# Optimization experiments

Hardware: AMD Instinct MI355X
Metric: run time of the kernel (lower is better)

Reference implementation:

```python
import jax, jax.numpy as jnp
import numpy as np
from jax import lax

B, T, E, H = 4096, 200, 64, 64
N_USER, N_ITEM = 100000, 100000
ATT_H1, ATT_H2 = 80, 40  # DIN attention MLP sizes
FCN_IN = 4 * E + H  # user + item + hist_sum + item*hist_sum + gru2 final state


def setup_inputs() -> dict:
    key = jax.random.key(0)
    ks = jax.random.split(key, 32)
    s = 0.1
    rn = lambda k, shp: (jax.random.normal(k, shp, dtype=jnp.float32) * s)
    u = jax.random.randint(ks[0], (B,), 0, N_USER)
    i = jax.random.randint(ks[1], (B,), 0, N_ITEM)
    hist_i = jax.random.randint(ks[2], (B, T), 0, N_ITEM)
    sl = jax.random.randint(ks[3], (B,), 1, T + 1)
    mask = (jnp.arange(T)[None, :] < sl[:, None]).astype(jnp.float32)
    inp = dict(u=u, i=i, hist_i=hist_i, mask=mask)
    inp.update(
        item_emb_w=rn(ks[4], (N_ITEM, E)),
        user_emb_w=rn(ks[5], (N_USER, E)),
        # GRU1 (input dim E, hidden H): gates [r,z] fused, candidate separate (TF GRUCell layout)
        gru1_Wg=rn(ks[6], (E, 2 * H)), gru1_Ug=rn(ks[7], (H, 2 * H)), gru1_bg=jnp.zeros((2 * H,), jnp.float32),
        gru1_Wc=rn(ks[8], (E, H)), gru1_Uc=rn(ks[9], (H, H)), gru1_bc=jnp.zeros((H,), jnp.float32),
        # DIN attention MLP over [q, k, q-k, q*k]
        Wa1=rn(ks[10], (4 * H, ATT_H1)), ba1=jnp.zeros((ATT_H1,), jnp.float32),
        Wa2=rn(ks[11], (ATT_H1, ATT_H2)), ba2=jnp.zeros((ATT_H2,), jnp.float32),
        Wa3=rn(ks[12], (ATT_H2, 1)), ba3=jnp.zeros((1,), jnp.float32),
        # GRU2 (input dim H, hidden H)
        gru2_Wg=rn(ks[13], (H, 2 * H)), gru2_Ug=rn(ks[14], (H, 2 * H)), gru2_bg=jnp.zeros((2 * H,), jnp.float32),
        gru2_Wc=rn(ks[15], (H, H)), gru2_Uc=rn(ks[16], (H, H)), gru2_bc=jnp.zeros((H,), jnp.float32),
        # fcn_net: dense(2E) -> prelu -> dense(40) -> prelu -> dense(1)
        W1=rn(ks[17], (FCN_IN, 2 * E)), b1=jnp.zeros((2 * E,), jnp.float32), p1=jnp.full((2 * E,), 0.25, jnp.float32),
        W2=rn(ks[18], (2 * E, 40)), b2=jnp.zeros((40,), jnp.float32), p2=jnp.full((40,), 0.25, jnp.float32),
        W3=rn(ks[19], (40, 1)), b3=jnp.zeros((1,), jnp.float32),
    )
    return inp


def _gru(x, mask, Wg, Ug, bg, Wc, Uc, bc):
    """TF GRUCell semantics; mask freezes state past sequence length. x: [B,T,D]."""
    xg = jnp.einsum('btd,dh->bth', x, Wg) + bg  # precompute input projections
    xc = jnp.einsum('btd,dh->bth', x, Wc) + bc
    h0 = jnp.zeros((x.shape[0], Uc.shape[0]), dtype=x.dtype)

    def step(h, inp):
        xg_t, xc_t, m = inp
        r, z = jnp.split(jax.nn.sigmoid(xg_t + h @ Ug), 2, axis=-1)
        c = jnp.tanh(xc_t + (r * h) @ Uc)
        h_new = z * h + (1.0 - z) * c
        h = m[:, None] * h_new + (1.0 - m[:, None]) * h
        return h, h

    hT, hs = lax.scan(step, h0, (xg.transpose(1, 0, 2), xc.transpose(1, 0, 2), mask.T))
    return jnp.transpose(hs, (1, 0, 2)), hT  # [B,T,H], [B,H]


def _prelu(x, a):
    return jnp.where(x >= 0, x, a * x)


def reference(u, i, hist_i, mask, item_emb_w, user_emb_w,
              gru1_Wg, gru1_Ug, gru1_bg, gru1_Wc, gru1_Uc, gru1_bc,
              Wa1, ba1, Wa2, ba2, Wa3, ba3,
              gru2_Wg, gru2_Ug, gru2_bg, gru2_Wc, gru2_Uc, gru2_bc,
              W1, b1, p1, W2, b2, p2, W3, b3):
    item_eb = item_emb_w[i]            # [B,E]
    user_eb = user_emb_w[u]            # [B,E]
    hist_eb = item_emb_w[hist_i]       # [B,T,E]
    hist_sum = jnp.sum(hist_eb, axis=1)  # original uses unmasked reduce_sum

    # GRU encoder over history
    rnn1, _ = _gru(hist_eb, mask, gru1_Wg, gru1_Ug, gru1_bg, gru1_Wc, gru1_Uc, gru1_bc)

    # DIN-style attention: target item queries GRU1 states
    q = jnp.broadcast_to(item_eb[:, None, :], rnn1.shape)  # [B,T,H] (E==H)
    din = jnp.concatenate([q, rnn1, q - rnn1, q * rnn1], axis=-1)  # [B,T,4H]
    d1 = jax.nn.sigmoid(din @ Wa1 + ba1)
    d2 = jax.nn.sigmoid(d1 @ Wa2 + ba2)
    scores = (d2 @ Wa3 + ba3)[..., 0]  # [B,T]
    scores = jnp.where(mask > 0, scores, -1e9)
    alpha = jax.nn.softmax(scores, axis=-1)  # [B,T]

    # second GRU over attention-weighted states
    att_in = rnn1 * alpha[..., None]
    _, final2 = _gru(att_in, mask, gru2_Wg, gru2_Ug, gru2_bg, gru2_Wc, gru2_Uc, gru2_bc)

    # fcn_net on concatenated features
    inp = jnp.concatenate([user_eb, item_eb, hist_sum, item_eb * hist_sum, final2], axis=-1)
    h1 = _prelu(inp @ W1 + b1, p1)
    h2 = _prelu(h1 @ W2 + b2, p2)
    logits = (h2 @ W3 + b3)[:, 0]  # [B]
    return logits
```

## Files before the change

### kernel.cpp

```cpp
#include <hip/hip_runtime.h>

#define BB 4096
#define TT 200

typedef unsigned short u16;
typedef unsigned int   u32;
typedef unsigned short u16x8 __attribute__((ext_vector_type(8)));
typedef short s16x8 __attribute__((ext_vector_type(8)));
typedef float f32x4 __attribute__((ext_vector_type(4)));

__device__ __forceinline__ float bf2f(u16 u){ union{unsigned u; float f;} v; v.u=((unsigned)u)<<16; return v.f; }
__device__ __forceinline__ u16 f2bf(float f){ union{float f; unsigned u;} v; v.f=f; unsigned r=v.u + 0x7FFFu + ((v.u>>16)&1u); return (u16)(r>>16); }
__device__ __forceinline__ float sigm(float x){ return 1.0f/(1.0f+__expf(-x)); }
__device__ __forceinline__ float tanh_(float x){ return 1.0f - 2.0f/(1.0f+__expf(2.0f*x)); }

#define MFMA16(a,b,c) __builtin_amdgcn_mfma_f32_16x16x32_bf16((a),(b),(c),0,0,0)

__device__ __forceinline__ void split8(const f32x4 a, const f32x4 b, s16x8 &hi, s16x8 &lo){
#pragma unroll
  for (int j=0;j<4;j++){
    float v=a[j]; u16 h=(u16)(__float_as_uint(v)>>16);
    hi[j]=(short)h; lo[j]=(short)f2bf(v-bf2f(h));
    v=b[j]; h=(u16)(__float_as_uint(v)>>16);
    hi[j+4]=(short)h; lo[j+4]=(short)f2bf(v-bf2f(h));
  }
}


__global__ void hist_sum_kernel(const int* __restrict__ hist, const float* __restrict__ emb,
                                float* __restrict__ hs){
  int tid = blockIdx.x*256 + threadIdx.x;
  int b = tid>>3, cg = (tid&7)*8;
  float acc[8];
#pragma unroll
  for (int j=0;j<8;j++) acc[j]=0.0f;
  for (int t=0;t<TT;t++){
    int idx = hist[(size_t)b*TT+t];
    f32x4 v0=*(const f32x4*)(emb+(size_t)idx*64+cg);
    f32x4 v1=*(const f32x4*)(emb+(size_t)idx*64+cg+4);
#pragma unroll
    for (int j=0;j<4;j++){ acc[j]+=v0[j]; acc[j+4]+=v1[j]; }
  }
#pragma unroll
  for (int j=0;j<8;j++) hs[(size_t)b*64+cg+j]=acc[j];
}

__global__ __launch_bounds__(256,1) void scan1_kernel(
    const int* __restrict__ hist, const float* __restrict__ mask, const float* __restrict__ emb,
    const float* __restrict__ Wg, const float* __restrict__ Ug, const float* __restrict__ bg,
    const float* __restrict__ Wc, const float* __restrict__ Uc, const float* __restrict__ bc,
    int* __restrict__ len_g, u16* __restrict__ rnn1)
{
  __shared__ float h1buf[16][68];
  __shared__ float pbuf [16][68];
  __shared__ int   lenL [16];
  const int tid=threadIdx.x;
  const int w=tid>>6, lane=tid&63, q=lane>>4, mm=lane&15;
  const int g=blockIdx.x, b0=g*16, pb_m=b0+mm;

  if (w==0){
    int cnt=0;
    for (int t=q*50;t<q*50+50;t++) cnt += (mask[(size_t)pb_m*TT+t]!=0.0f);
    cnt += __shfl_xor(cnt,16);
    cnt += __shfl_xor(cnt,32);
    if (lane<16){ lenL[lane]=cnt; len_g[b0+lane]=cnt; }
  }
  for (int ii=tid; ii<16*68; ii+=256) (&h1buf[0][0])[ii]=0.0f;
  __syncthreads();

  int lenq[4];
#pragma unroll
  for (int r=0;r<4;r++) lenq[r]=lenL[q*4+r];
  int maxlen=1;
  for (int i=0;i<16;i++) maxlen=(lenL[i]>maxlen)?lenL[i]:maxlen;

  const int nr=16*w+mm, nz=64+16*w+mm;
  s16x8 wgr[4], wgz[4], wcf[4];
#pragma unroll
  for (int c=0;c<4;c++){
    s16x8 fr,fz,fc;
#pragma unroll
    for (int j=0;j<8;j++){
      int k=32*c+q*8+j;
      fr[j]=(short)f2bf((k<64)?Wg[(size_t)k*128+nr]:Ug[(size_t)(k-64)*128+nr]);
      fz[j]=(short)f2bf((k<64)?Wg[(size_t)k*128+nz]:Ug[(size_t)(k-64)*128+nz]);
      fc[j]=(short)f2bf((k<64)?Wc[(size_t)k*64+nr]:Uc[(size_t)(k-64)*64+nr]);
    }
    wgr[c]=fr; wgz[c]=fz; wcf[c]=fc;
  }
  const float bgr=bg[nr], bgz=bg[nz], bcv=bc[nr];

  auto load_x=[&](int t, s16x8 &a0, s16x8 &a1){
    int idx = hist[(size_t)pb_m*TT+t];
    const float* p=emb+(size_t)idx*64;
    f32x4 v0=*(const f32x4*)(p+q*8),    v1=*(const f32x4*)(p+q*8+4);
    f32x4 v2=*(const f32x4*)(p+32+q*8), v3=*(const f32x4*)(p+32+q*8+4);
    s16x8 t0,t1;
#pragma unroll
    for (int j=0;j<4;j++){
      t0[j]=(short)f2bf(v0[j]); t0[j+4]=(short)f2bf(v1[j]);
      t1[j]=(short)f2bf(v2[j]); t1[j+4]=(short)f2bf(v3[j]);
    }
    a0=t0; a1=t1;
  };

  s16x8 xf0,xf1;
  load_x(0,xf0,xf1);
  for (int t=0;t<maxlen;t++){
    s16x8 nx0,nx1;
    { int tn=(t+1<maxlen)?(t+1):(maxlen-1); load_x(tn,nx0,nx1); }

    f32x4 hA0=*(const f32x4*)&h1buf[mm][q*8];
    f32x4 hA1=*(const f32x4*)&h1buf[mm][q*8+4];
    f32x4 hB0=*(const f32x4*)&h1buf[mm][32+q*8];
    f32x4 hB1=*(const f32x4*)&h1buf[mm][32+q*8+4];
    s16x8 hhi0,hlo0,hhi1,hlo1;
    split8(hA0,hA1,hhi0,hlo0);
    split8(hB0,hB1,hhi1,hlo1);

    f32x4 ar={0.0f,0.0f,0.0f,0.0f}, az={0.0f,0.0f,0.0f,0.0f};
    ar=MFMA16(xf0 ,wgr[0],ar); az=MFMA16(xf0 ,wgz[0],az);
    ar=MFMA16(xf1 ,wgr[1],ar); az=MFMA16(xf1 ,wgz[1],az);
    ar=MFMA16(hhi0,wgr[2],ar); az=MFMA16(hhi0,wgz[2],az);
    ar=MFMA16(hhi1,wgr[3],ar); az=MFMA16(hhi1,wgz[3],az);
    ar=MFMA16(hlo0,wgr[2],ar); az=MFMA16(hlo0,wgz[2],az);
    ar=MFMA16(hlo1,wgr[3],ar); az=MFMA16(hlo1,wgz[3],az);

    float zs[4], hv[4];
#pragma unroll
    for (int r=0;r<4;r++){
      float rg=sigm(ar[r]+bgr);
      float hp=h1buf[q*4+r][16*w+mm];
      hv[r]=hp;
      pbuf[q*4+r][16*w+mm]=rg*hp;
      zs[r]=sigm(az[r]+bgz);
    }
    __syncthreads();

    f32x4 pA0=*(const f32x4*)&pbuf[mm][q*8];
    f32x4 pA1=*(const f32x4*)&pbuf[mm][q*8+4];
    f32x4 pB0=*(const f32x4*)&pbuf[mm][32+q*8];
    f32x4 pB1=*(const f32x4*)&pbuf[mm][32+q*8+4];
    s16x8 phi0,plo0,phi1,plo1;
    split8(pA0,pA1,phi0,plo0);
    split8(pB0,pB1,phi1,plo1);

    f32x4 ac={0.0f,0.0f,0.0f,0.0f};
    ac=MFMA16(xf0 ,wcf[0],ac);
    ac=MFMA16(xf1 ,wcf[1],ac);
    ac=MFMA16(phi0,wcf[2],ac);
    ac=MFMA16(phi1,wcf[3],ac);
    ac=MFMA16(plo0,wcf[2],ac);
    ac=MFMA16(plo1,wcf[3],ac);
#pragma unroll
    for (int r=0;r<4;r++){
      float c=tanh_(ac[r]+bcv);
      float z=zs[r];
      float hn=z*hv[r]+(1.0f-z)*c;
      if (t>=lenq[r]) hn=hv[r];
      h1buf[q*4+r][16*w+mm]=hn;
      rnn1[((size_t)(b0+q*4+r)*TT+t)*64 + 16*w+mm]=f2bf(hn);
    }
    __syncthreads();
    xf0=nx0; xf1=nx1;
  }
}

__global__ __launch_bounds__(64,1) void attn_kernel(
    const int* __restrict__ iidx, const float* __restrict__ emb, const u16* __restrict__ rnn1,
    const float* __restrict__ Wa1, const float* __restrict__ ba1,
    const float* __restrict__ Wa2, const float* __restrict__ ba2,
    const float* __restrict__ Wa3, const float* __restrict__ ba3,
    const int* __restrict__ len_g, float* __restrict__ scores)
{
  __shared__ u16 d1buf[16][104];
  const int lane=threadIdx.x, q=lane>>4, mm=lane&15;
  const int b=blockIdx.x;
  const int L=len_g[b];

  s16x8 w1k[5][2], wd[5][2];
#pragma unroll
  for (int nt=0;nt<5;nt++)
#pragma unroll
    for (int c=0;c<2;c++){
      s16x8 f1,f2;
#pragma unroll
      for (int j=0;j<8;j++){
        int k=32*c+q*8+j, n=16*nt+mm;
        f1[j]=(short)f2bf(Wa1[(size_t)(64+k)*80+n] - Wa1[(size_t)(128+k)*80+n]);
        f2[j]=(short)f2bf(Wa1[(size_t)(192+k)*80+n]);
      }
      w1k[nt][c]=f1; wd[nt][c]=f2;
    }
  s16x8 w2f[3][3];
#pragma unroll
  for (int nt=0;nt<3;nt++)
#pragma unroll
    for (int c=0;c<3;c++){
      s16x8 f;
#pragma unroll
      for (int j=0;j<8;j++){
        int k=32*c+q*8+j, n=16*nt+mm;
        f[j]=(short)((k<80 && n<40)?f2bf(Wa2[(size_t)k*40+n]):0);
      }
      w2f[nt][c]=f;
    }
  float ba2v[3], w3v[3];
#pragma unroll
  for (int nt=0;nt<3;nt++){ int n=16*nt+mm; ba2v[nt]=(n<40)?ba2[n]:0.0f; w3v[nt]=(n<40)?Wa3[n]:0.0f; }
  const float ba3v=ba3[0];

  const int ib=iidx[b];
  float qv0[8], qv1[8];
  s16x8 aq0,aq1;
#pragma unroll
  for (int j=0;j<8;j++){
    qv0[j]=emb[(size_t)ib*64+q*8+j];
    qv1[j]=emb[(size_t)ib*64+32+q*8+j];
    aq0[j]=(short)f2bf(qv0[j]); aq1[j]=(short)f2bf(qv1[j]);
  }
  float pre[5];
#pragma unroll
  for (int nt=0;nt<5;nt++){
    int n=16*nt+mm;
    s16x8 bp0,bp1;
#pragma unroll
    for (int j=0;j<8;j++){
      int k=q*8+j, k2=32+q*8+j;
      bp0[j]=(short)f2bf(Wa1[(size_t)k *80+n]+Wa1[(size_t)(128+k )*80+n]);
      bp1[j]=(short)f2bf(Wa1[(size_t)k2*80+n]+Wa1[(size_t)(128+k2)*80+n]);
    }
    f32x4 a={0.0f,0.0f,0.0f,0.0f};
    a=MFMA16(aq0,bp0,a); a=MFMA16(aq1,bp1,a);
    pre[nt]=a[0]+ba1[n];
  }

  for (int ii=lane; ii<16*104; ii+=64) (&d1buf[0][0])[ii]=0;
  __syncthreads();

  const int nch=(L+15)>>4;
  for (int ch=0; ch<nch; ch++){
    int t0=ch*16;
    size_t base=((size_t)b*TT + t0+mm)*64;
    s16x8 kf0=*(const s16x8*)(rnn1+base+q*8);
    s16x8 kf1=*(const s16x8*)(rnn1+base+32+q*8);
    s16x8 kq0,kq1;
#pragma unroll
    for (int j=0;j<8;j++){
      kq0[j]=(short)f2bf(bf2f((u16)kf0[j])*qv0[j]);
      kq1[j]=(short)f2bf(bf2f((u16)kf1[j])*qv1[j]);
    }
    f32x4 acc[5];
#pragma unroll
    for (int nt=0;nt<5;nt++){
      f32x4 a={pre[nt],pre[nt],pre[nt],pre[nt]};
      a=MFMA16(kf0,w1k[nt][0],a); a=MFMA16(kf1,w1k[nt][1],a);
      a=MFMA16(kq0,wd[nt][0],a);  a=MFMA16(kq1,wd[nt][1],a);
      acc[nt]=a;
    }
#pragma unroll
    for (int nt=0;nt<5;nt++)
#pragma unroll
      for (int r=0;r<4;r++)
        d1buf[q*4+r][16*nt+mm]=f2bf(sigm(acc[nt][r]));
    __syncthreads();
    s16x8 a0=*(const s16x8*)&d1buf[mm][q*8];
    s16x8 a1=*(const s16x8*)&d1buf[mm][32+q*8];
    s16x8 a2=*(const s16x8*)&d1buf[mm][64+q*8];
    f32x4 acc2[3];
#pragma unroll
    for (int nt=0;nt<3;nt++){
      f32x4 a={0.0f,0.0f,0.0f,0.0f};
      a=MFMA16(a0,w2f[nt][0],a); a=MFMA16(a1,w2f[nt][1],a); a=MFMA16(a2,w2f[nt][2],a);
      acc2[nt]=a;
    }
    float part[4];
#pragma unroll
    for (int r=0;r<4;r++){
      float s=0.0f;
#pragma unroll
      for (int nt=0;nt<3;nt++) s+=sigm(acc2[nt][r]+ba2v[nt])*w3v[nt];
      part[r]=s;
    }
#pragma unroll
    for (int d=1;d<16;d<<=1)
#pragma unroll
      for (int r=0;r<4;r++) part[r]+=__shfl_xor(part[r],d);
    if (mm==0){
#pragma unroll
      for (int r=0;r<4;r++){ int t=t0+q*4+r; if (t<TT) scores[(size_t)b*TT+t]=part[r]+ba3v; }
    }
    __syncthreads();
  }
}

__global__ __launch_bounds__(64,1) void softmax_kernel(const int* __restrict__ len_g, float* __restrict__ sc){
  const int b=blockIdx.x, lane=threadIdx.x;
  const int L=len_g[b];
  float mx=-3e38f;
  for (int t=lane;t<L;t+=64) mx=fmaxf(mx,sc[(size_t)b*TT+t]);
#pragma unroll
  for (int d=1;d<64;d<<=1) mx=fmaxf(mx,__shfl_xor(mx,d));
  float sm=0.0f;
  for (int t=lane;t<L;t+=64) sm+=__expf(sc[(size_t)b*TT+t]-mx);
#pragma unroll
  for (int d=1;d<64;d<<=1) sm+=__shfl_xor(sm,d);
  float inv=1.0f/sm;
  for (int t=lane;t<TT;t+=64){
    float v=(t<L)?__expf(sc[(size_t)b*TT+t]-mx)*inv:0.0f;
    sc[(size_t)b*TT+t]=v;
  }
}

__global__ __launch_bounds__(256,1) void scan2_kernel(
    const u16* __restrict__ rnn1, const float* __restrict__ alpha, const int* __restrict__ len_g,
    const float* __restrict__ Wg, const float* __restrict__ Ug, const float* __restrict__ bg,
    const float* __restrict__ Wc, const float* __restrict__ Uc, const float* __restrict__ bc,
    float* __restrict__ f2)
{
  __shared__ float h2buf[16][68];
  __shared__ float pbuf [16][68];
  __shared__ int   lenL [16];
  const int tid=threadIdx.x;
  const int w=tid>>6, lane=tid&63, q=lane>>4, mm=lane&15;
  const int g=blockIdx.x, b0=g*16, pb_m=b0+mm;

  if (tid<16) lenL[tid]=len_g[b0+tid];
  for (int ii=tid; ii<16*68; ii+=256) (&h2buf[0][0])[ii]=0.0f;
  __syncthreads();

  int lenq[4];
#pragma unroll
  for (int r=0;r<4;r++) lenq[r]=lenL[q*4+r];
  int maxlen=1;
  for (int i=0;i<16;i++) maxlen=(lenL[i]>maxlen)?lenL[i]:maxlen;

  const int nr=16*w+mm, nz=64+16*w+mm;
  s16x8 wgr[4], wgz[4], wcf[4];
#pragma unroll
  for (int c=0;c<4;c++){
    s16x8 fr,fz,fc;
#pragma unroll
    for (int j=0;j<8;j++){
      int k=32*c+q*8+j;
      fr[j]=(short)f2bf((k<64)?Wg[(size_t)k*128+nr]:Ug[(size_t)(k-64)*128+nr]);
      fz[j]=(short)f2bf((k<64)?Wg[(size_t)k*128+nz]:Ug[(size_t)(k-64)*128+nz]);
      fc[j]=(short)f2bf((k<64)?Wc[(size_t)k*64+nr]:Uc[(size_t)(k-64)*64+nr]);
    }
    wgr[c]=fr; wgz[c]=fz; wcf[c]=fc;
  }
  const float bgr=bg[nr], bgz=bg[nz], bcv=bc[nr];

  auto load_x=[&](int t, s16x8 &a0, s16x8 &a1){
    size_t base=((size_t)pb_m*TT+t)*64;
    u16x8 k0=*(const u16x8*)(rnn1+base+q*8);
    u16x8 k1=*(const u16x8*)(rnn1+base+32+q*8);
    float al=alpha[(size_t)pb_m*TT+t];
    s16x8 t0,t1;
#pragma unroll
    for (int j=0;j<8;j++){
      t0[j]=(short)f2bf(bf2f(k0[j])*al);
      t1[j]=(short)f2bf(bf2f(k1[j])*al);
    }
    a0=t0; a1=t1;
  };

  s16x8 xf0,xf1;
  load_x(0,xf0,xf1);
  for (int t=0;t<maxlen;t++){
    s16x8 nx0,nx1;
    { int tn=(t+1<maxlen)?(t+1):(maxlen-1); load_x(tn,nx0,nx1); }

    f32x4 hA0=*(const f32x4*)&h2buf[mm][q*8];
    f32x4 hA1=*(const f32x4*)&h2buf[mm][q*8+4];
    f32x4 hB0=*(const f32x4*)&h2buf[mm][32+q*8];
    f32x4 hB1=*(const f32x4*)&h2buf[mm][32+q*8+4];
    s16x8 hhi0,hlo0,hhi1,hlo1;
    split8(hA0,hA1,hhi0,hlo0);
    split8(hB0,hB1,hhi1,hlo1);

    f32x4 ar={0.0f,0.0f,0.0f,0.0f}, az={0.0f,0.0f,0.0f,0.0f};
    ar=MFMA16(xf0 ,wgr[0],ar); az=MFMA16(xf0 ,wgz[0],az);
    ar=MFMA16(xf1 ,wgr[1],ar); az=MFMA16(xf1 ,wgz[1],az);
    ar=MFMA16(hhi0,wgr[2],ar); az=MFMA16(hhi0,wgz[2],az);
    ar=MFMA16(hhi1,wgr[3],ar); az=MFMA16(hhi1,wgz[3],az);
    ar=MFMA16(hlo0,wgr[2],ar); az=MFMA16(hlo0,wgz[2],az);
    ar=MFMA16(hlo1,wgr[3],ar); az=MFMA16(hlo1,wgz[3],az);

    float zs[4], hv[4];
#pragma unroll
    for (int r=0;r<4;r++){
      float rg=sigm(ar[r]+bgr);
      float hp=h2buf[q*4+r][16*w+mm];
      hv[r]=hp;
      pbuf[q*4+r][16*w+mm]=rg*hp;
      zs[r]=sigm(az[r]+bgz);
    }
    __syncthreads();

    f32x4 pA0=*(const f32x4*)&pbuf[mm][q*8];
    f32x4 pA1=*(const f32x4*)&pbuf[mm][q*8+4];
    f32x4 pB0=*(const f32x4*)&pbuf[mm][32+q*8];
    f32x4 pB1=*(const f32x4*)&pbuf[mm][32+q*8+4];
    s16x8 phi0,plo0,phi1,plo1;
    split8(pA0,pA1,phi0,plo0);
    split8(pB0,pB1,phi1,plo1);

    f32x4 ac={0.0f,0.0f,0.0f,0.0f};
    ac=MFMA16(xf0 ,wcf[0],ac);
    ac=MFMA16(xf1 ,wcf[1],ac);
    ac=MFMA16(phi0,wcf[2],ac);
    ac=MFMA16(phi1,wcf[3],ac);
    ac=MFMA16(plo0,wcf[2],ac);
    ac=MFMA16(plo1,wcf[3],ac);
#pragma unroll
    for (int r=0;r<4;r++){
      float c=tanh_(ac[r]+bcv);
      float z=zs[r];
      float hn=z*hv[r]+(1.0f-z)*c;
      if (t>=lenq[r]) hn=hv[r];
      h2buf[q*4+r][16*w+mm]=hn;
    }
    __syncthreads();
    xf0=nx0; xf1=nx1;
  }

#pragma unroll
  for (int r=0;r<4;r++)
    f2[(size_t)(b0+q*4+r)*64 + 16*w+mm]=h2buf[q*4+r][16*w+mm];
}

__global__ __launch_bounds__(64,1) void fcn_kernel(
    const int* __restrict__ uidx, const int* __restrict__ iidx,
    const float* __restrict__ uemb, const float* __restrict__ emb,
    const float* __restrict__ hs, const float* __restrict__ f2,
    const float* __restrict__ Wf1, const float* __restrict__ fb1, const float* __restrict__ fp1,
    const float* __restrict__ Wf2, const float* __restrict__ fb2, const float* __restrict__ fp2,
    const float* __restrict__ Wf3, const float* __restrict__ fb3,
    float* __restrict__ out)
{
  __shared__ float inL[16][320];
  __shared__ u16   h1L[16][128];
  __shared__ float h2o[16][40];
  const int lane=threadIdx.x, q=lane>>4, mm=lane&15;
  const int b0=blockIdx.x*16;

  {
    int row=lane>>2, sub=lane&3;
    int b=b0+row;
    int ub=uidx[b], ibv=iidx[b];
    for (int c=sub*80;c<sub*80+80;c++){
      int seg=c>>6, f=c&63; float v;
      if      (seg==0) v=uemb[(size_t)ub*64+f];
      else if (seg==1) v=emb[(size_t)ibv*64+f];
      else if (seg==2) v=hs[(size_t)b*64+f];
      else if (seg==3) v=emb[(size_t)ibv*64+f]*hs[(size_t)b*64+f];
      else             v=f2[(size_t)b*64+f];
      inL[row][c]=v;
    }
  }
  __syncthreads();

  {
    f32x4 acc1[8];
#pragma unroll
    for (int nt=0;nt<8;nt++) acc1[nt]=f32x4{0.0f,0.0f,0.0f,0.0f};
#pragma unroll
    for (int kc=0;kc<10;kc++){
      s16x8 af;
#pragma unroll
      for (int j=0;j<8;j++) af[j]=(short)f2bf(inL[mm][32*kc+q*8+j]);
#pragma unroll
      for (int nt=0;nt<8;nt++){
        s16x8 bfr;
#pragma unroll
        for (int j=0;j<8;j++) bfr[j]=(short)f2bf(Wf1[(size_t)(32*kc+q*8+j)*128 + 16*nt+mm]);
        acc1[nt]=MFMA16(af,bfr,acc1[nt]);
      }
    }
#pragma unroll
    for (int nt=0;nt<8;nt++)
#pragma unroll
      for (int r=0;r<4;r++){
        int col=16*nt+mm, row=q*4+r;
        float x=acc1[nt][r]+fb1[col];
        float pp=fp1[col];
        h1L[row][col]=f2bf((x>=0.0f)?x:pp*x);
      }
  }
  __syncthreads();

  {
    f32x4 acc2[3];
#pragma unroll
    for (int nt=0;nt<3;nt++) acc2[nt]=f32x4{0.0f,0.0f,0.0f,0.0f};
#pragma unroll
    for (int kc=0;kc<4;kc++){
      s16x8 af=*(const s16x8*)&h1L[mm][32*kc+q*8];
#pragma unroll
      for (int nt=0;nt<3;nt++){
        s16x8 bfr;
#pragma unroll
        for (int j=0;j<8;j++){
          int k=32*kc+q*8+j, n=16*nt+mm;
          bfr[j]=(short)((n<40)?f2bf(Wf2[(size_t)k*40+n]):0);
        }
        acc2[nt]=MFMA16(af,bfr,acc2[nt]);
      }
    }
#pragma unroll
    for (int nt=0;nt<3;nt++)
#pragma unroll
      for (int r=0;r<4;r++){
        int col=16*nt+mm, row=q*4+r;
        if (col<40){
          float x=acc2[nt][r]+fb2[col];
          float pp=fp2[col];
          h2o[row][col]=(x>=0.0f)?x:pp*x;
        }
      }
  }
  __syncthreads();

  {
    int row=lane>>2, sub=lane&3;
    float s=0.0f;
    for (int k=sub;k<40;k+=4) s+=h2o[row][k]*Wf3[k];
    s+=__shfl_xor(s,1); s+=__shfl_xor(s,2);
    if (sub==0) out[b0+row]=s+fb3[0];
  }
}

template<bool F32>
__global__ __launch_bounds__(64,1) void dien_mega_kernel(
    const int* __restrict__ uidx, const int* __restrict__ iidx,
    const int* __restrict__ hist, const void* __restrict__ mask,
    const void* __restrict__ emb,  const void* __restrict__ uemb,
    const void* __restrict__ W1g, const void* __restrict__ U1g, const void* __restrict__ g1bg,
    const void* __restrict__ W1c, const void* __restrict__ U1c, const void* __restrict__ g1bc,
    const void* __restrict__ Wa1, const void* __restrict__ ba1,
    const void* __restrict__ Wa2, const void* __restrict__ ba2,
    const void* __restrict__ Wa3, const void* __restrict__ ba3,
    const void* __restrict__ W2g, const void* __restrict__ U2g, const void* __restrict__ g2bg,
    const void* __restrict__ W2c, const void* __restrict__ U2c, const void* __restrict__ g2bc,
    const void* __restrict__ Wf1, const void* __restrict__ fb1, const void* __restrict__ fp1,
    const void* __restrict__ Wf2, const void* __restrict__ fb2, const void* __restrict__ fp2,
    const void* __restrict__ Wf3, const void* __restrict__ fb3,
    void* __restrict__ outp)
{
  auto LF=[&](const void* p, size_t i)->float {
    return F32 ? ((const float*)p)[i] : bf2f(((const u16*)p)[i]);
  };
  auto LB=[&](const void* p, size_t i)->u16 {
    return F32 ? f2bf(((const float*)p)[i]) : ((const u16*)p)[i];
  };
  auto FR8=[&](const void* p, size_t off)->s16x8 {
    s16x8 f;
    if (F32){
      const float* pp=(const float*)p+off;
      f32x4 a=*(const f32x4*)pp, b=*(const f32x4*)(pp+4);
#pragma unroll
      for (int j=0;j<4;j++){ f[j]=(short)f2bf(a[j]); f[j+4]=(short)f2bf(b[j]); }
    } else {
      f=*(const s16x8*)((const u16*)p+off);
    }
    return f;
  };

  __shared__ float h1buf[16][68];
  __shared__ float h2buf[16][68];
  __shared__ float pbuf [16][68];
  __shared__ u16   d1buf[16][104];
  __shared__ u16   scL  [16][200];
  __shared__ float hsL  [16][64];
  __shared__ s16x8 u2gL [16][64];
  __shared__ s16x8 u2cL [ 8][64];
  __shared__ float h2o  [16][40];
  __shared__ u16   ueL  [16][64];
  __shared__ u16   ieL  [16][64];
  __shared__ int   lenL [16];

  const int lane=threadIdx.x, q=lane>>4, mm=lane&15;
// ... 442 lines not shown
        f32x4 a={0.0f,0.0f,0.0f,0.0f};
        a=MFMA16(af0 ,wc2x[nt][0],a);
        a=MFMA16(af1 ,wc2x[nt][1],a);
        a=MFMA16(phi0,wh0,a);
        a=MFMA16(phi1,wh1,a);
        a=MFMA16(plo0,wh0,a);
        a=MFMA16(plo1,wh1,a);
        ca[nt]=a;
      }
#pragma unroll
      for (int nt=0;nt<4;nt++)
#pragma unroll
        for (int r=0;r<4;r++){
          float c=tanh_(ca[nt][r]+b2cv[nt]);
          float z=zs[nt][r];
          float hn=z*hv[nt][r]+(1.0f-z)*c;
          if (t>=lenq[r]) hn=hv[nt][r];
          h2buf[q*4+r][16*nt+mm]=hn;
        }
      __syncthreads();
    }

    xf0=nx0; xf1=nx1;
  }

  {
    int row=lane>>2, c0=(lane&3)*16;
    int ub=uidx[b0+row], ibv=iidx[b0+row];
#pragma unroll
    for (int j=0;j<16;j++){
      ueL[row][c0+j]=LB(uemb,(size_t)ub*64+c0+j);
      ieL[row][c0+j]=LB(emb ,(size_t)ibv*64+c0+j);
    }
  }
  __syncthreads();

  {
    f32x4 acc1[8];
#pragma unroll
    for (int nt=0;nt<8;nt++) acc1[nt]=f32x4{0.0f,0.0f,0.0f,0.0f};
#pragma unroll
    for (int kc=0;kc<10;kc++){
      const int seg=kc>>1, off=(kc&1)*32+q*8;
      s16x8 af;
#pragma unroll
      for (int j=0;j<8;j++){
        int f=off+j;
        u16 v;
        if      (seg==0) v=ueL[mm][f];
        else if (seg==1) v=ieL[mm][f];
        else if (seg==2) v=f2bf(hsL[mm][f]);
        else if (seg==3) v=f2bf(bf2f(ieL[mm][f])*hsL[mm][f]);
        else             v=f2bf(h2buf[mm][f]);
        af[j]=(short)v;
      }
#pragma unroll
      for (int nt=0;nt<8;nt++){
        s16x8 bfr;
#pragma unroll
        for (int j=0;j<8;j++) bfr[j]=(short)LB(Wf1,(size_t)(32*kc+q*8+j)*128 + 16*nt+mm);
        acc1[nt]=MFMA16(af,bfr,acc1[nt]);
      }
    }
    __syncthreads();
#pragma unroll
    for (int nt=0;nt<8;nt++)
#pragma unroll
      for (int r=0;r<4;r++){
        int col=16*nt+mm, row=q*4+r;
        float x=acc1[nt][r]+LF(fb1,col);
        float pp=LF(fp1,col);
        scL[row][col]=f2bf((x>=0.0f)?x:pp*x);
      }
  }
  __syncthreads();

  {
    f32x4 acc2[3];
#pragma unroll
    for (int nt=0;nt<3;nt++) acc2[nt]=f32x4{0.0f,0.0f,0.0f,0.0f};
#pragma unroll
    for (int kc=0;kc<4;kc++){
      s16x8 af=*(const s16x8*)&scL[mm][32*kc+q*8];
#pragma unroll
      for (int nt=0;nt<3;nt++){
        s16x8 bfr;
#pragma unroll
        for (int j=0;j<8;j++){
          int k=32*kc+q*8+j, n=16*nt+mm;
          bfr[j]=(short)((n<40)?LB(Wf2,(size_t)k*40+n):0);
        }
        acc2[nt]=MFMA16(af,bfr,acc2[nt]);
      }
    }
#pragma unroll
    for (int nt=0;nt<3;nt++)
#pragma unroll
      for (int r=0;r<4;r++){
        int col=16*nt+mm, row=q*4+r;
        if (col<40){
          float x=acc2[nt][r]+LF(fb2,col);
          float pp=LF(fp2,col);
          h2o[row][col]=(x>=0.0f)?x:pp*x;
        }
      }
  }
  __syncthreads();

  {
    int row=lane>>2, sub=lane&3;
    float s=0.0f;
    for (int k=sub;k<40;k+=4) s+=h2o[row][k]*LF(Wf3,k);
    s+=__shfl_xor(s,1); s+=__shfl_xor(s,2);
    if (sub==0){
      float v=s+LF(fb3,0);
      if (F32) ((float*)outp)[b0+row]=v;
      else     ((u16*) outp)[b0+row]=f2bf(v);
    }
  }
}

extern "C" void kernel_launch(void* const* d_in, const int* in_sizes, int n_in,
                              void* d_out, int out_size, void* d_ws, size_t ws_size,
                              hipStream_t stream)
{
  (void)in_sizes; (void)n_in; (void)out_size;
  const int* u    =(const int*)d_in[0];
  const int* it   =(const int*)d_in[1];
  const int* hist =(const int*)d_in[2];
  const float* mask=(const float*)d_in[3];
  const float* item_emb=(const float*)d_in[4];
  const float* user_emb=(const float*)d_in[5];
  const float* g1Wg=(const float*)d_in[6],  *g1Ug=(const float*)d_in[7],  *g1bg=(const float*)d_in[8];
  const float* g1Wc=(const float*)d_in[9],  *g1Uc=(const float*)d_in[10], *g1bc=(const float*)d_in[11];
  const float* Wa1=(const float*)d_in[12], *ba1=(const float*)d_in[13];
  const float* Wa2=(const float*)d_in[14], *ba2=(const float*)d_in[15];
  const float* Wa3=(const float*)d_in[16], *ba3=(const float*)d_in[17];
  const float* g2Wg=(const float*)d_in[18], *g2Ug=(const float*)d_in[19], *g2bg=(const float*)d_in[20];
  const float* g2Wc=(const float*)d_in[21], *g2Uc=(const float*)d_in[22], *g2bc=(const float*)d_in[23];
  const float* W1=(const float*)d_in[24], *b1=(const float*)d_in[25], *p1=(const float*)d_in[26];
  const float* W2=(const float*)d_in[27], *b2=(const float*)d_in[28], *p2=(const float*)d_in[29];
  const float* W3=(const float*)d_in[30], *b3=(const float*)d_in[31];

  const size_t sz_rnn1  =(size_t)BB*TT*64*2;
  const size_t sz_scores=(size_t)BB*TT*4;
  const size_t sz_len   =(size_t)BB*4;
  const size_t sz_hs    =(size_t)BB*64*4;
  const size_t sz_f2    =(size_t)BB*64*4;
  const size_t NEED = sz_rnn1+sz_scores+sz_len+sz_hs+sz_f2 + 1024;

  if (ws_size >= NEED){
    char* ws=(char*)d_ws;
    u16*   rnn1  =(u16*)  ws;                    ws+=sz_rnn1;
    float* scores=(float*)ws;                    ws+=sz_scores;
    int*   len_g =(int*)  ws;                    ws+=sz_len;
    float* hs    =(float*)ws;                    ws+=sz_hs;
    float* f2    =(float*)ws;

    hist_sum_kernel<<<BB*8/256,256,0,stream>>>(hist, item_emb, hs);
    scan1_kernel   <<<BB/16,   256,0,stream>>>(hist, mask, item_emb,
                                               g1Wg,g1Ug,g1bg,g1Wc,g1Uc,g1bc,
                                               len_g, rnn1);
    attn_kernel    <<<BB,       64,0,stream>>>(it, item_emb, rnn1,
                                               Wa1,ba1,Wa2,ba2,Wa3,ba3,
                                               len_g, scores);
    softmax_kernel <<<BB,       64,0,stream>>>(len_g, scores);
    scan2_kernel   <<<BB/16,   256,0,stream>>>(rnn1, scores, len_g,
                                               g2Wg,g2Ug,g2bg,g2Wc,g2Uc,g2bc,
                                               f2);
    fcn_kernel     <<<BB/16,    64,0,stream>>>(u, it, user_emb, item_emb, hs, f2,
                                               W1,b1,p1,W2,b2,p2,W3,b3,
                                               (float*)d_out);
  } else {
    dien_mega_kernel<true><<<BB/16, 64, 0, stream>>>(
        u, it, hist, mask, item_emb, user_emb,
        g1Wg,g1Ug,g1bg,g1Wc,g1Uc,g1bc,
        Wa1,ba1,Wa2,ba2,Wa3,ba3,
        g2Wg,g2Ug,g2bg,g2Wc,g2Uc,g2bc,
        W1,b1,p1,W2,b2,p2,W3,b3,
        d_out);
  }
}
```

Baseline: 909.9 us.

## Fuse hist-sum into GRU1 scan, softmax into attention, use packed bf16 converts

Removes the separate hist_sum kernel by having wave 0 of scan1 accumulate history embeddings while it loads GRU inputs, then finish the tail past maxlen. Folds the softmax into the attention kernel by keeping scores in shared memory and writing alpha directly, which drops a launch and a global round trip. Replaces scalar float-to-bf16 rounding with a packed two-element conversion builtin when it is available, cutting ALU work in the serial scan loops. In exchange, wave 0 of scan1 carries extra accumulation work and registers, which may add to the critical path.

Result: slower. 1.078 ms (+18.5%).

```diff
diff --git a/kernel.cpp b/kernel.cpp
--- a/kernel.cpp
+++ b/kernel.cpp
@@ -9,47 +9,53 @@
 typedef short s16x8 __attribute__((ext_vector_type(8)));
 typedef float f32x4 __attribute__((ext_vector_type(4)));
 
+#if defined(__has_builtin)
+#if __has_builtin(__builtin_amdgcn_cvt_pk_bf16_f32)
+#define HAVE_PKBF 1
+typedef __bf16 bf16x2_t __attribute__((ext_vector_type(2)));
+#endif
+#endif
+
 __device__ __forceinline__ float bf2f(u16 u){ union{unsigned u; float f;} v; v.u=((unsigned)u)<<16; return v.f; }
-__device__ __forceinline__ u16 f2bf(float f){ union{float f; unsigned u;} v; v.f=f; unsigned r=v.u + 0x7FFFu + ((v.u>>16)&1u); return (u16)(r>>16); }
+
+__device__ __forceinline__ u32 cvt2(float a, float b){
+#ifdef HAVE_PKBF
+  bf16x2_t v=__builtin_amdgcn_cvt_pk_bf16_f32(a,b);
+  return __builtin_bit_cast(u32,v);
+#else
+  union{float f; u32 u;} x,y; x.f=a; y.f=b;
+  u32 ra=x.u+0x7FFFu+((x.u>>16)&1u);
+  u32 rb=y.u+0x7FFFu+((y.u>>16)&1u);
+  return (ra>>16)|(rb&0xFFFF0000u);
+#endif
+}
+__device__ __forceinline__ u16 f2bf(float f){ return (u16)cvt2(f,0.0f); }
 __device__ __forceinline__ float sigm(float x){ return 1.0f/(1.0f+__expf(-x)); }
 __device__ __forceinline__ float tanh_(float x){ return 1.0f - 2.0f/(1.0f+__expf(2.0f*x)); }
 
 #define MFMA16(a,b,c) __builtin_amdgcn_mfma_f32_16x16x32_bf16((a),(b),(c),0,0,0)
 
 __device__ __forceinline__ void split8(const f32x4 a, const f32x4 b, s16x8 &hi, s16x8 &lo){
-#pragma unroll
-  for (int j=0;j<4;j++){
-    float v=a[j]; u16 h=(u16)(__float_as_uint(v)>>16);
-    hi[j]=(short)h; lo[j]=(short)f2bf(v-bf2f(h));
-    v=b[j]; h=(u16)(__float_as_uint(v)>>16);
-    hi[j+4]=(short)h; lo[j+4]=(short)f2bf(v-bf2f(h));
+  u32* hp=(u32*)&hi; u32* lp=(u32*)&lo;
+#pragma unroll
+  for (int j=0;j<2;j++){
+    float x0=a[2*j], x1=a[2*j+1];
+    u32 h=cvt2(x0,x1);
+    hp[j]=h;
+    lp[j]=cvt2(x0-__uint_as_float(h<<16), x1-__uint_as_float(h&0xFFFF0000u));
+    float y0=b[2*j], y1=b[2*j+1];
+    u32 g=cvt2(y0,y1);
+    hp[j+2]=g;
+    lp[j+2]=cvt2(y0-__uint_as_float(g<<16), y1-__uint_as_float(g&0xFFFF0000u));
   }
 }
 
-
-__global__ void hist_sum_kernel(const int* __restrict__ hist, const float* __restrict__ emb,
-                                float* __restrict__ hs){
-  int tid = blockIdx.x*256 + threadIdx.x;
-  int b = tid>>3, cg = (tid&7)*8;
-  float acc[8];
-#pragma unroll
-  for (int j=0;j<8;j++) acc[j]=0.0f;
-  for (int t=0;t<TT;t++){
-    int idx = hist[(size_t)b*TT+t];
-    f32x4 v0=*(const f32x4*)(emb+(size_t)idx*64+cg);
-    f32x4 v1=*(const f32x4*)(emb+(size_t)idx*64+cg+4);
-#pragma unroll
-    for (int j=0;j<4;j++){ acc[j]+=v0[j]; acc[j+4]+=v1[j]; }
-  }
-#pragma unroll
-  for (int j=0;j<8;j++) hs[(size_t)b*64+cg+j]=acc[j];
-}
 
 __global__ __launch_bounds__(256,1) void scan1_kernel(
     const int* __restrict__ hist, const float* __restrict__ mask, const float* __restrict__ emb,
     const float* __restrict__ Wg, const float* __restrict__ Ug, const float* __restrict__ bg,
     const float* __restrict__ Wc, const float* __restrict__ Uc, const float* __restrict__ bc,
-    int* __restrict__ len_g, u16* __restrict__ rnn1)
+    int* __restrict__ len_g, u16* __restrict__ rnn1, float* __restrict__ hs)
 {
   __shared__ float h1buf[16][68];
   __shared__ float pbuf [16][68];
@@ -90,25 +96,31 @@
   }
   const float bgr=bg[nr], bgz=bg[nz], bcv=bc[nr];
 
-  auto load_x=[&](int t, s16x8 &a0, s16x8 &a1){
+  float hsA[8], hsB[8];
+#pragma unroll
+  for (int j=0;j<8;j++){ hsA[j]=0.0f; hsB[j]=0.0f; }
+
+  auto load_x=[&](int t, s16x8 &a0, s16x8 &a1, bool acc){
     int idx = hist[(size_t)pb_m*TT+t];
     const float* p=emb+(size_t)idx*64;
     f32x4 v0=*(const f32x4*)(p+q*8),    v1=*(const f32x4*)(p+q*8+4);
     f32x4 v2=*(const f32x4*)(p+32+q*8), v3=*(const f32x4*)(p+32+q*8+4);
-    s16x8 t0,t1;
-#pragma unroll
-    for (int j=0;j<4;j++){
-      t0[j]=(short)f2bf(v0[j]); t0[j+4]=(short)f2bf(v1[j]);
-      t1[j]=(short)f2bf(v2[j]); t1[j+4]=(short)f2bf(v3[j]);
-    }
-    a0=t0; a1=t1;
+    if (w==0 && acc){
+#pragma unroll
+      for (int j=0;j<4;j++){ hsA[j]+=v0[j]; hsA[j+4]+=v1[j]; hsB[j]+=v2[j]; hsB[j+4]+=v3[j]; }
+    }
+    u32* p0=(u32*)&a0; u32* p1=(u32*)&a1;
+    p0[0]=cvt2(v0[0],v0[1]); p0[1]=cvt2(v0[2],v0[3]);
+    p0[2]=cvt2(v1[0],v1[1]); p0[3]=cvt2(v1[2],v1[3]);
+    p1[0]=cvt2(v2[0],v2[1]); p1[1]=cvt2(v2[2],v2[3]);
+    p1[2]=cvt2(v3[0],v3[1]); p1[3]=cvt2(v3[2],v3[3]);
   };
 
   s16x8 xf0,xf1;
-  load_x(0,xf0,xf1);
+  load_x(0,xf0,xf1,true);
   for (int t=0;t<maxlen;t++){
     s16x8 nx0,nx1;
-    { int tn=(t+1<maxlen)?(t+1):(maxlen-1); load_x(tn,nx0,nx1); }
+    { bool more=(t+1<maxlen); int tn=more?(t+1):(maxlen-1); load_x(tn,nx0,nx1,more); }
 
     f32x4 hA0=*(const f32x4*)&h1buf[mm][q*8];
     f32x4 hA1=*(const f32x4*)&h1buf[mm][q*8+4];
@@ -164,6 +176,23 @@
     __syncthreads();
     xf0=nx0; xf1=nx1;
   }
+
+  if (w==0){
+    for (int t=maxlen;t<TT;t++){
+      int idx = hist[(size_t)pb_m*TT+t];
+      const float* p=emb+(size_t)idx*64;
+      f32x4 v0=*(const f32x4*)(p+q*8),    v1=*(const f32x4*)(p+q*8+4);
+      f32x4 v2=*(const f32x4*)(p+32+q*8), v3=*(const f32x4*)(p+32+q*8+4);
+#pragma unroll
+      for (int j=0;j<4;j++){ hsA[j]+=v0[j]; hsA[j+4]+=v1[j]; hsB[j]+=v2[j]; hsB[j+4]+=v3[j]; }
+    }
+    f32x4 o0={hsA[0],hsA[1],hsA[2],hsA[3]}, o1={hsA[4],hsA[5],hsA[6],hsA[7]};
+    f32x4 o2={hsB[0],hsB[1],hsB[2],hsB[3]}, o3={hsB[4],hsB[5],hsB[6],hsB[7]};
+    *(f32x4*)(hs+(size_t)pb_m*64+q*8)   =o0;
+    *(f32x4*)(hs+(size_t)pb_m*64+q*8+4) =o1;
+    *(f32x4*)(hs+(size_t)pb_m*64+32+q*8)  =o2;
+    *(f32x4*)(hs+(size_t)pb_m*64+32+q*8+4)=o3;
+  }
 }
 
 __global__ __launch_bounds__(64,1) void attn_kernel(
@@ -171,9 +200,10 @@
     const float* __restrict__ Wa1, const float* __restrict__ ba1,
     const float* __restrict__ Wa2, const float* __restrict__ ba2,
     const float* __restrict__ Wa3, const float* __restrict__ ba3,
-    const int* __restrict__ len_g, float* __restrict__ scores)
+    const int* __restrict__ len_g, float* __restrict__ alph)
 {
   __shared__ u16 d1buf[16][104];
+  __shared__ float scS[208];
   const int lane=threadIdx.x, q=lane>>4, mm=lane&15;
   const int b=blockIdx.x;
   const int L=len_g[b];
@@ -236,6 +266,7 @@
   }
 
   for (int ii=lane; ii<16*104; ii+=64) (&d1buf[0][0])[ii]=0;
+  for (int t=lane;t<208;t+=64) scS[t]=-1e9f;
   __syncthreads();
 
   const int nch=(L+15)>>4;
@@ -245,10 +276,12 @@
     s16x8 kf0=*(const s16x8*)(rnn1+base+q*8);
     s16x8 kf1=*(const s16x8*)(rnn1+base+32+q*8);
     s16x8 kq0,kq1;
-#pragma unroll
-    for (int j=0;j<8;j++){
-      kq0[j]=(short)f2bf(bf2f((u16)kf0[j])*qv0[j]);
-      kq1[j]=(short)f2bf(bf2f((u16)kf1[j])*qv1[j]);
+    { u32* kp0=(u32*)&kq0; u32* kp1=(u32*)&kq1;
+#pragma unroll
+      for (int j=0;j<4;j++){
+        kp0[j]=cvt2(bf2f((u16)kf0[2*j])*qv0[2*j], bf2f((u16)kf0[2*j+1])*qv0[2*j+1]);
+        kp1[j]=cvt2(bf2f((u16)kf1[2*j])*qv1[2*j], bf2f((u16)kf1[2*j+1])*qv1[2*j+1]);
+      }
     }
     f32x4 acc[5];
 #pragma unroll
@@ -288,27 +321,23 @@
       for (int r=0;r<4;r++) part[r]+=__shfl_xor(part[r],d);
     if (mm==0){
 #pragma unroll
-      for (int r=0;r<4;r++){ int t=t0+q*4+r; if (t<TT) scores[(size_t)b*TT+t]=part[r]+ba3v; }
+      for (int r=0;r<4;r++){ int t=t0+q*4+r; scS[t]=(t<L)?(part[r]+ba3v):-1e9f; }
     }
     __syncthreads();
   }
-}
-
-__global__ __launch_bounds__(64,1) void softmax_kernel(const int* __restrict__ len_g, float* __restrict__ sc){
-  const int b=blockIdx.x, lane=threadIdx.x;
-  const int L=len_g[b];
+
   float mx=-3e38f;
-  for (int t=lane;t<L;t+=64) mx=fmaxf(mx,sc[(size_t)b*TT+t]);
+  for (int t=lane;t<TT;t+=64) mx=fmaxf(mx,scS[t]);
 #pragma unroll
   for (int d=1;d<64;d<<=1) mx=fmaxf(mx,__shfl_xor(mx,d));
   float sm=0.0f;
-  for (int t=lane;t<L;t+=64) sm+=__expf(sc[(size_t)b*TT+t]-mx);
+  for (int t=lane;t<TT;t+=64) sm+=__expf(scS[t]-mx);
 #pragma unroll
   for (int d=1;d<64;d<<=1) sm+=__shfl_xor(sm,d);
   float inv=1.0f/sm;
   for (int t=lane;t<TT;t+=64){
-    float v=(t<L)?__expf(sc[(size_t)b*TT+t]-mx)*inv:0.0f;
-    sc[(size_t)b*TT+t]=v;
+    float v=(t<L)?__expf(scS[t]-mx)*inv:0.0f;
+    alph[(size_t)b*TT+t]=v;
   }
 }
 
@@ -356,13 +385,12 @@
     u16x8 k0=*(const u16x8*)(rnn1+base+q*8);
     u16x8 k1=*(const u16x8*)(rnn1+base+32+q*8);
     float al=alpha[(size_t)pb_m*TT+t];
-    s16x8 t0,t1;
-#pragma unroll
-    for (int j=0;j<8;j++){
-      t0[j]=(short)f2bf(bf2f(k0[j])*al);
-      t1[j]=(short)f2bf(bf2f(k1[j])*al);
-    }
-    a0=t0; a1=t1;
+    u32* p0=(u32*)&a0; u32* p1=(u32*)&a1;
+#pragma unroll
+    for (int j=0;j<4;j++){
+      p0[j]=cvt2(bf2f(k0[2*j])*al, bf2f(k0[2*j+1])*al);
+      p1[j]=cvt2(bf2f(k1[2*j])*al, bf2f(k1[2*j+1])*al);
+    }
   };
 
   s16x8 xf0,xf1;
@@ -1176,25 +1204,23 @@
   if (ws_size >= NEED){
     char* ws=(char*)d_ws;
     u16*   rnn1  =(u16*)  ws;                    ws+=sz_rnn1;
-    float* scores=(float*)ws;                    ws+=sz_scores;
+    float* alpha =(float*)ws;                    ws+=sz_scores;
     int*   len_g =(int*)  ws;                    ws+=sz_len;
     float* hs    =(float*)ws;                    ws+=sz_hs;
     float* f2    =(float*)ws;
 
-    hist_sum_kernel<<<BB*8/256,256,0,stream>>>(hist, item_emb, hs);
-    scan1_kernel   <<<BB/16,   256,0,stream>>>(hist, mask, item_emb,
-                                               g1Wg,g1Ug,g1bg,g1Wc,g1Uc,g1bc,
-                                               len_g, rnn1);
-    attn_kernel    <<<BB,       64,0,stream>>>(it, item_emb, rnn1,
-                                               Wa1,ba1,Wa2,ba2,Wa3,ba3,
-                                               len_g, scores);
-    softmax_kernel <<<BB,       64,0,stream>>>(len_g, scores);
-    scan2_kernel   <<<BB/16,   256,0,stream>>>(rnn1, scores, len_g,
-                                               g2Wg,g2Ug,g2bg,g2Wc,g2Uc,g2bc,
-                                               f2);
-    fcn_kernel     <<<BB/16,    64,0,stream>>>(u, it, user_emb, item_emb, hs, f2,
-                                               W1,b1,p1,W2,b2,p2,W3,b3,
-                                               (float*)d_out);
+    scan1_kernel<<<BB/16, 256, 0, stream>>>(hist, mask, item_emb,
+                                            g1Wg,g1Ug,g1bg,g1Wc,g1Uc,g1bc,
+                                            len_g, rnn1, hs);
+    attn_kernel <<<BB,     64, 0, stream>>>(it, item_emb, rnn1,
+                                            Wa1,ba1,Wa2,ba2,Wa3,ba3,
+                                            len_g, alpha);
+    scan2_kernel<<<BB/16, 256, 0, stream>>>(rnn1, alpha, len_g,
+                                            g2Wg,g2Ug,g2bg,g2Wc,g2Uc,g2bc,
+                                            f2);
+    fcn_kernel  <<<BB/16,  64, 0, stream>>>(u, it, user_emb, item_emb, hs, f2,
+                                            W1,b1,p1,W2,b2,p2,W3,b3,
+                                            (float*)d_out);
   } else {
     dien_mega_kernel<true><<<BB/16, 64, 0, stream>>>(
         u, it, hist, mask, item_emb, user_emb,
```

## Halve batch per scan block to double grid and fuse softmax into attention

Applied to the files above, without the earlier changes.

Both GRU scan kernels now handle 8 batch rows per block instead of 16. The MFMA M-dimension of 16 is filled by duplicating the 8 rows, and the grid doubles to 512 blocks with launch bounds allowing 2 blocks per CU, so the latency-bound sequential scans get more parallelism across CUs. Half the MFMA work is redundant. The separate softmax kernel is removed: attention scores stay in LDS and the softmax is computed at the end of attn_kernel, which saves one launch and a global round trip of the scores.

After: 1.175 ms. 1.29x slower.

```diff
diff --git a/kernel.cpp b/kernel.cpp
--- a/kernel.cpp
+++ b/kernel.cpp
@@ -45,7 +45,7 @@
   for (int j=0;j<8;j++) hs[(size_t)b*64+cg+j]=acc[j];
 }
 
-__global__ __launch_bounds__(256,1) void scan1_kernel(
+__global__ __launch_bounds__(256,2) void scan1_kernel(
     const int* __restrict__ hist, const float* __restrict__ mask, const float* __restrict__ emb,
     const float* __restrict__ Wg, const float* __restrict__ Ug, const float* __restrict__ bg,
     const float* __restrict__ Wc, const float* __restrict__ Uc, const float* __restrict__ bc,
@@ -56,14 +56,15 @@
   __shared__ int   lenL [16];
   const int tid=threadIdx.x;
   const int w=tid>>6, lane=tid&63, q=lane>>4, mm=lane&15;
-  const int g=blockIdx.x, b0=g*16, pb_m=b0+mm;
+  const int g=blockIdx.x, b0=g*8, pb_m=b0+(mm&7);
 
   if (w==0){
     int cnt=0;
     for (int t=q*50;t<q*50+50;t++) cnt += (mask[(size_t)pb_m*TT+t]!=0.0f);
     cnt += __shfl_xor(cnt,16);
     cnt += __shfl_xor(cnt,32);
-    if (lane<16){ lenL[lane]=cnt; len_g[b0+lane]=cnt; }
+    if (lane<16) lenL[lane]=cnt;
+    if (lane<8)  len_g[b0+lane]=cnt;
   }
   for (int ii=tid; ii<16*68; ii+=256) (&h1buf[0][0])[ii]=0.0f;
   __syncthreads();
@@ -72,7 +73,7 @@
 #pragma unroll
   for (int r=0;r<4;r++) lenq[r]=lenL[q*4+r];
   int maxlen=1;
-  for (int i=0;i<16;i++) maxlen=(lenL[i]>maxlen)?lenL[i]:maxlen;
+  for (int i=0;i<8;i++) maxlen=(lenL[i]>maxlen)?lenL[i]:maxlen;
 
   const int nr=16*w+mm, nz=64+16*w+mm;
   s16x8 wgr[4], wgz[4], wcf[4];
@@ -159,7 +160,7 @@
       float hn=z*hv[r]+(1.0f-z)*c;
       if (t>=lenq[r]) hn=hv[r];
       h1buf[q*4+r][16*w+mm]=hn;
-      rnn1[((size_t)(b0+q*4+r)*TT+t)*64 + 16*w+mm]=f2bf(hn);
+      if (q<2) rnn1[((size_t)(b0+q*4+r)*TT+t)*64 + 16*w+mm]=f2bf(hn);
     }
     __syncthreads();
     xf0=nx0; xf1=nx1;
@@ -171,9 +172,10 @@
     const float* __restrict__ Wa1, const float* __restrict__ ba1,
     const float* __restrict__ Wa2, const float* __restrict__ ba2,
     const float* __restrict__ Wa3, const float* __restrict__ ba3,
-    const int* __restrict__ len_g, float* __restrict__ scores)
+    const int* __restrict__ len_g, float* __restrict__ alph)
 {
   __shared__ u16 d1buf[16][104];
+  __shared__ float scS[208];
   const int lane=threadIdx.x, q=lane>>4, mm=lane&15;
   const int b=blockIdx.x;
   const int L=len_g[b];
@@ -236,6 +238,7 @@
   }
 
   for (int ii=lane; ii<16*104; ii+=64) (&d1buf[0][0])[ii]=0;
+  for (int t=lane;t<208;t+=64) scS[t]=-1e9f;
   __syncthreads();
 
   const int nch=(L+15)>>4;
@@ -288,31 +291,27 @@
       for (int r=0;r<4;r++) part[r]+=__shfl_xor(part[r],d);
     if (mm==0){
 #pragma unroll
-      for (int r=0;r<4;r++){ int t=t0+q*4+r; if (t<TT) scores[(size_t)b*TT+t]=part[r]+ba3v; }
+      for (int r=0;r<4;r++){ int t=t0+q*4+r; scS[t]=(t<L)?(part[r]+ba3v):-1e9f; }
     }
     __syncthreads();
   }
-}
-
-__global__ __launch_bounds__(64,1) void softmax_kernel(const int* __restrict__ len_g, float* __restrict__ sc){
-  const int b=blockIdx.x, lane=threadIdx.x;
-  const int L=len_g[b];
+
   float mx=-3e38f;
-  for (int t=lane;t<L;t+=64) mx=fmaxf(mx,sc[(size_t)b*TT+t]);
+  for (int t=lane;t<TT;t+=64) mx=fmaxf(mx,scS[t]);
 #pragma unroll
   for (int d=1;d<64;d<<=1) mx=fmaxf(mx,__shfl_xor(mx,d));
   float sm=0.0f;
-  for (int t=lane;t<L;t+=64) sm+=__expf(sc[(size_t)b*TT+t]-mx);
+  for (int t=lane;t<TT;t+=64) sm+=__expf(scS[t]-mx);
 #pragma unroll
   for (int d=1;d<64;d<<=1) sm+=__shfl_xor(sm,d);
   float inv=1.0f/sm;
   for (int t=lane;t<TT;t+=64){
-    float v=(t<L)?__expf(sc[(size_t)b*TT+t]-mx)*inv:0.0f;
-    sc[(size_t)b*TT+t]=v;
+    float v=(t<L)?__expf(scS[t]-mx)*inv:0.0f;
+    alph[(size_t)b*TT+t]=v;
   }
 }
 
-__global__ __launch_bounds__(256,1) void scan2_kernel(
+__global__ __launch_bounds__(256,2) void scan2_kernel(
     const u16* __restrict__ rnn1, const float* __restrict__ alpha, const int* __restrict__ len_g,
     const float* __restrict__ Wg, const float* __restrict__ Ug, const float* __restrict__ bg,
     const float* __restrict__ Wc, const float* __restrict__ Uc, const float* __restrict__ bc,
@@ -323,9 +322,9 @@
   __shared__ int   lenL [16];
   const int tid=threadIdx.x;
   const int w=tid>>6, lane=tid&63, q=lane>>4, mm=lane&15;
-  const int g=blockIdx.x, b0=g*16, pb_m=b0+mm;
-
-  if (tid<16) lenL[tid]=len_g[b0+tid];
+  const int g=blockIdx.x, b0=g*8, pb_m=b0+(mm&7);
+
+  if (tid<16) lenL[tid]=len_g[b0+(tid&7)];
   for (int ii=tid; ii<16*68; ii+=256) (&h2buf[0][0])[ii]=0.0f;
   __syncthreads();
 
@@ -333,7 +332,7 @@
 #pragma unroll
   for (int r=0;r<4;r++) lenq[r]=lenL[q*4+r];
   int maxlen=1;
-  for (int i=0;i<16;i++) maxlen=(lenL[i]>maxlen)?lenL[i]:maxlen;
+  for (int i=0;i<8;i++) maxlen=(lenL[i]>maxlen)?lenL[i]:maxlen;
 
   const int nr=16*w+mm, nz=64+16*w+mm;
   s16x8 wgr[4], wgz[4], wcf[4];
@@ -427,7 +426,7 @@
 
 #pragma unroll
   for (int r=0;r<4;r++)
-    f2[(size_t)(b0+q*4+r)*64 + 16*w+mm]=h2buf[q*4+r][16*w+mm];
+    if (q<2) f2[(size_t)(b0+q*4+r)*64 + 16*w+mm]=h2buf[q*4+r][16*w+mm];
 }
 
 __global__ __launch_bounds__(64,1) void fcn_kernel(
@@ -1176,25 +1175,24 @@
   if (ws_size >= NEED){
     char* ws=(char*)d_ws;
     u16*   rnn1  =(u16*)  ws;                    ws+=sz_rnn1;
-    float* scores=(float*)ws;                    ws+=sz_scores;
+    float* alpha =(float*)ws;                    ws+=sz_scores;
     int*   len_g =(int*)  ws;                    ws+=sz_len;
     float* hs    =(float*)ws;                    ws+=sz_hs;
     float* f2    =(float*)ws;
 
     hist_sum_kernel<<<BB*8/256,256,0,stream>>>(hist, item_emb, hs);
-    scan1_kernel   <<<BB/16,   256,0,stream>>>(hist, mask, item_emb,
-                                               g1Wg,g1Ug,g1bg,g1Wc,g1Uc,g1bc,
-                                               len_g, rnn1);
-    attn_kernel    <<<BB,       64,0,stream>>>(it, item_emb, rnn1,
-                                               Wa1,ba1,Wa2,ba2,Wa3,ba3,
-                                               len_g, scores);
-    softmax_kernel <<<BB,       64,0,stream>>>(len_g, scores);
-    scan2_kernel   <<<BB/16,   256,0,stream>>>(rnn1, scores, len_g,
-                                               g2Wg,g2Ug,g2bg,g2Wc,g2Uc,g2bc,
-                                               f2);
-    fcn_kernel     <<<BB/16,    64,0,stream>>>(u, it, user_emb, item_emb, hs, f2,
-                                               W1,b1,p1,W2,b2,p2,W3,b3,
-                                               (float*)d_out);
+    scan1_kernel<<<BB/8,  256, 0, stream>>>(hist, mask, item_emb,
+                                            g1Wg,g1Ug,g1bg,g1Wc,g1Uc,g1bc,
+                                            len_g, rnn1);
+    attn_kernel <<<BB,     64, 0, stream>>>(it, item_emb, rnn1,
+                                            Wa1,ba1,Wa2,ba2,Wa3,ba3,
+                                            len_g, alpha);
+    scan2_kernel<<<BB/8,  256, 0, stream>>>(rnn1, alpha, len_g,
+                                            g2Wg,g2Ug,g2bg,g2Wc,g2Uc,g2bc,
+                                            f2);
+    fcn_kernel  <<<BB/16,  64, 0, stream>>>(u, it, user_emb, item_emb, hs, f2,
+                                            W1,b1,p1,W2,b2,p2,W3,b3,
+                                            (float*)d_out);
   } else {
     dien_mega_kernel<true><<<BB/16, 64, 0, stream>>>(
         u, it, hist, mask, item_emb, user_emb,
```
